# Kernel tuning notes

Measured on AMD Instinct MI355X. Metric: run time of the kernel, lower is better.

## Reference

```python
import jax, jax.numpy as jnp
import numpy as np

D_MODEL = 1024
NHEAD = 16


def unitnorm(v):
    # F.normalize(v, dim=-1): v / max(||v||_2, 1e-12)
    n = jnp.sqrt(jnp.sum(v * v, axis=-1, keepdims=True))
    return v / jnp.maximum(n, 1e-12)


def setup_inputs() -> dict:
    key = jax.random.key(0)
    ks = jax.random.split(key, 14)
    d = D_MODEL
    sc = 1.0 / np.sqrt(d)
    inp = jax.random.normal(ks[0], (2048, 8, d), dtype=jnp.float32)
    def lin(kw, kb, out_dim):
        W = jax.random.uniform(kw, (out_dim, d), minval=-sc, maxval=sc, dtype=jnp.float32)
        b = jax.random.uniform(kb, (out_dim,), minval=-sc, maxval=sc, dtype=jnp.float32)
        return W, b
    Wq_w, Wq_b = lin(ks[1], ks[2], d)
    Wk_w, Wk_b = lin(ks[3], ks[4], d)
    Wv_w, Wv_b = lin(ks[5], ks[6], d)
    Wo_w, Wo_b = lin(ks[7], ks[8], d)
    Ww_w, Ww_b = lin(ks[9], ks[10], NHEAD)
    Wr_w, Wr_b = lin(ks[11], ks[12], NHEAD)
    return {"inp": inp, "Wq_w": Wq_w, "Wq_b": Wq_b, "Wk_w": Wk_w, "Wk_b": Wk_b,
            "Wv_w": Wv_w, "Wv_b": Wv_b, "Wo_w": Wo_w, "Wo_b": Wo_b,
            "Ww_w": Ww_w, "Ww_b": Ww_b, "Wr_w": Wr_w, "Wr_b": Wr_b}


def reference(inp, Wq_w, Wq_b, Wk_w, Wk_b, Wv_w, Wv_b, Wo_w, Wo_b, Ww_w, Ww_b, Wr_w, Wr_b):
    src = inp  # src=None path
    S, B, d = inp.shape
    n = NHEAD
    # torch Linear: x @ W.T + b
    k = (src @ Wk_w.T + Wk_b).reshape(S, B, n, -1)
    v = (src @ Wv_w.T + Wv_b).reshape(S, B, n, -1)
    q = (inp @ Wq_w.T + Wq_b).reshape(S, B, n, -1)
    k = unitnorm(k)
    q = unitnorm(q)
    w = jax.nn.sigmoid(src @ Ww_w.T + Ww_b)            # [S,B,n]
    A = jnp.einsum('sbnq,sbnv->bnvq', k, v * w[:, :, :, None])
    r = jax.nn.sigmoid(inp @ Wr_w.T + Wr_b)            # [S,B,n]
    out = jnp.einsum('sbnq,bnvq->sbnv', q, A) * r[:, :, :, None]
    out = out.reshape(S, B, d)
    out = out @ Wo_w.T + Wo_b
    return (out, A)
```

## Files before the change

### kernel.cpp

```cpp
#include <hip/hip_runtime.h>
#include <cstdint>
#include <cstddef>


typedef __bf16 bf16x8 __attribute__((ext_vector_type(8)));
typedef float  f32x4  __attribute__((ext_vector_type(4)));
typedef unsigned short u16x8 __attribute__((ext_vector_type(8)));
typedef unsigned short u16x4 __attribute__((ext_vector_type(4)));

#define ROWS 16384
#define DM   1024

__device__ __forceinline__ unsigned short f2bf(float f) {
  unsigned int u = __builtin_bit_cast(unsigned int, f);
  u += 0x7FFFu + ((u >> 16) & 1u);
  return (unsigned short)(u >> 16);
}
__device__ __forceinline__ float bf2f(unsigned short h) {
  unsigned int u = ((unsigned int)h) << 16;
  return __builtin_bit_cast(float, u);
}
__device__ __forceinline__ float sigm(float x) { return 1.0f / (1.0f + __expf(-x)); }

__device__ __forceinline__ void gload_lds16(const void* g, void* l) {
  __builtin_amdgcn_global_load_lds((__attribute__((address_space(1))) void*)(g),
                                   (__attribute__((address_space(3))) void*)(l),
                                   16, 0, 0);
}

__global__ __launch_bounds__(256) void k_cast_x(const float* __restrict__ X,
                                                unsigned short* __restrict__ Xb) {
  size_t i = ((size_t)blockIdx.x * 256 + threadIdx.x) * 8;
  f32x4 a = *(const f32x4*)(X + i);
  f32x4 b = *(const f32x4*)(X + i + 4);
  u16x8 o;
  o[0] = f2bf(a[0]); o[1] = f2bf(a[1]); o[2] = f2bf(a[2]); o[3] = f2bf(a[3]);
  o[4] = f2bf(b[0]); o[5] = f2bf(b[1]); o[6] = f2bf(b[2]); o[7] = f2bf(b[3]);
  *(u16x8*)(Xb + i) = o;
}

__global__ __launch_bounds__(256) void k_pack_w(
    const float* __restrict__ Wq, const float* __restrict__ Wk, const float* __restrict__ Wv,
    const float* __restrict__ Wo, const float* __restrict__ Ww, const float* __restrict__ Wr,
    const float* __restrict__ bq, const float* __restrict__ bk, const float* __restrict__ bv,
    const float* __restrict__ bw, const float* __restrict__ br,
    unsigned short* __restrict__ Wpack, float* __restrict__ biasP,
    unsigned short* __restrict__ WRw, float* __restrict__ biasWR,
    unsigned short* __restrict__ Wob) {
  int r = blockIdx.x, t = threadIdx.x;
  const float* src; float bias = 0.0f; unsigned short* dst; float* bdst;
  if (r < 1024)      { src = Wq + (size_t)r * DM;          bias = bq[r];        dst = Wpack + (size_t)r * DM;          bdst = biasP + r; }
  else if (r < 2048) { src = Wk + (size_t)(r - 1024) * DM; bias = bk[r - 1024]; dst = Wpack + (size_t)r * DM;          bdst = biasP + r; }
  else if (r < 3072) { src = Wv + (size_t)(r - 2048) * DM; bias = bv[r - 2048]; dst = Wpack + (size_t)r * DM;          bdst = biasP + r; }
  else if (r < 3088) { src = Ww + (size_t)(r - 3072) * DM; bias = bw[r - 3072]; dst = WRw + (size_t)(r - 3072) * DM;   bdst = biasWR + (r - 3072); }
  else if (r < 3104) { src = Wr + (size_t)(r - 3088) * DM; bias = br[r - 3088]; dst = WRw + (size_t)(r - 3072) * DM;   bdst = biasWR + (r - 3072); }
  else               { src = Wo + (size_t)(r - 3104) * DM;                      dst = Wob + (size_t)(r - 3104) * DM;   bdst = nullptr; }
  int c = t * 4;
  f32x4 v = *(const f32x4*)(src + c);
  u16x4 o;
  o[0] = f2bf(v[0]); o[1] = f2bf(v[1]); o[2] = f2bf(v[2]); o[3] = f2bf(v[3]);
  *(u16x4*)(dst + c) = o;
  if (t == 0 && bdst) *bdst = bias;
}

__global__ __launch_bounds__(256) void k_wr(const unsigned short* __restrict__ Xb,
                                            const unsigned short* __restrict__ WRw,
                                            const float* __restrict__ biasWR,
                                            float* __restrict__ WRf) {
  __shared__ __bf16 sA[128 * 64];
  __shared__ __bf16 sB[32 * 64];
  int t = threadIdx.x, lane = t & 63, wid = t >> 6;
  int m0 = blockIdx.x * 128;
  int l15 = lane & 15, l4 = lane >> 4;
  f32x4 acc[2][2];
#pragma unroll
  for (int i = 0; i < 2; ++i)
#pragma unroll
    for (int j = 0; j < 2; ++j) acc[i][j] = (f32x4){0.f, 0.f, 0.f, 0.f};
  int srow = t >> 3, schunk = (t & 7) * 8;
  for (int kt = 0; kt < DM; kt += 64) {
#pragma unroll
    for (int c = 0; c < 4; ++c)
      gload_lds16(Xb + (size_t)(m0 + c * 32 + srow) * DM + kt + schunk,
                  (void*)(sA + c * 2048 + wid * 512));
    gload_lds16(WRw + (size_t)srow * DM + kt + schunk, (void*)(sB + wid * 512));
    __syncthreads();
#pragma unroll
    for (int ks = 0; ks < 2; ++ks) {
      bf16x8 fa[2], fb[2];
#pragma unroll
      for (int mi = 0; mi < 2; ++mi)
        fa[mi] = *(const bf16x8*)(sA + (wid * 32 + mi * 16 + l15) * 64 + (ks * 4 + l4) * 8);
#pragma unroll
      for (int ni = 0; ni < 2; ++ni)
        fb[ni] = *(const bf16x8*)(sB + (ni * 16 + l15) * 64 + (ks * 4 + l4) * 8);
#pragma unroll
      for (int mi = 0; mi < 2; ++mi)
#pragma unroll
        for (int ni = 0; ni < 2; ++ni)
          acc[mi][ni] = __builtin_amdgcn_mfma_f32_16x16x32_bf16(fa[mi], fb[ni], acc[mi][ni], 0, 0, 0);
    }
    __syncthreads();
  }
#pragma unroll
  for (int mi = 0; mi < 2; ++mi)
#pragma unroll
    for (int e = 0; e < 4; ++e) {
      int row = m0 + wid * 32 + mi * 16 + 4 * l4 + e;
#pragma unroll
      for (int ni = 0; ni < 2; ++ni)
        WRf[(size_t)row * 32 + ni * 16 + l15] = acc[mi][ni][e] + biasWR[ni * 16 + l15];
    }
}

__global__ __launch_bounds__(512, 2) void k_gemm_qkv3(
    const unsigned short* __restrict__ Xb, const unsigned short* __restrict__ Wpack,
    const float* __restrict__ biasP, const float* __restrict__ WRf,
    unsigned short* __restrict__ Qb, unsigned short* __restrict__ Kb,
    unsigned short* __restrict__ Vb) {
  __shared__ __bf16 sm[65536];
  const int t = threadIdx.x, lane = t & 63, w = t >> 6;
  const int wm = w >> 2, wn = w & 3;
  const int l15 = lane & 15, l4 = lane >> 4, l7 = lane & 7;
  int orig = blockIdx.x;
  int wg = (orig & 7) * 96 + (orig >> 3);
  const int m0 = (wg & 63) << 8;
  const int n0 = (wg >> 6) << 8;

  const int srow = t >> 3;
  const int schunk = ((t & 7) ^ (srow & 7)) * 8;
  const unsigned short* Asrc = Xb + (size_t)(m0 + srow) * DM + schunk;
  const unsigned short* Bsrc = Wpack + (size_t)(n0 + srow) * DM + schunk;

  f32x4 acc[8][4];
#pragma unroll
  for (int i = 0; i < 8; ++i)
#pragma unroll
    for (int j = 0; j < 4; ++j) acc[i][j] = (f32x4){0.f, 0.f, 0.f, 0.f};

#define STAGE256(P, kt)                                                            \
  do {                                                                             \
    _Pragma("unroll") for (int c = 0; c < 4; ++c)                                  \
      gload_lds16(Asrc + (size_t)c * 64 * DM + (kt),                               \
                  (void*)(sm + (P) * 32768 + c * 4096 + w * 512));                 \
    _Pragma("unroll") for (int c = 0; c < 4; ++c)                                  \
      gload_lds16(Bsrc + (size_t)c * 64 * DM + (kt),                               \
                  (void*)(sm + (P) * 32768 + 16384 + c * 4096 + w * 512));         \
  } while (0)

  STAGE256(0, 0);
  __syncthreads();
  for (int kt16 = 0; kt16 < 16; ++kt16) {
    int P = kt16 & 1;
    if (kt16 < 15) STAGE256(P ^ 1, (kt16 + 1) * 64);
    const __bf16* A0 = sm + P * 32768;
    const __bf16* B0 = A0 + 16384;
#pragma unroll
    for (int ks = 0; ks < 2; ++ks) {
      bf16x8 fa[8], fb[4];
      int ck = (((ks * 4 + l4) ^ l7) << 3);
#pragma unroll
      for (int mi = 0; mi < 8; ++mi)
        fa[mi] = *(const bf16x8*)(A0 + (wm * 128 + mi * 16 + l15) * 64 + ck);
#pragma unroll
      for (int ni = 0; ni < 4; ++ni)
        fb[ni] = *(const bf16x8*)(B0 + (wn * 64 + ni * 16 + l15) * 64 + ck);
#pragma unroll
      for (int mi = 0; mi < 8; ++mi)
#pragma unroll
        for (int ni = 0; ni < 4; ++ni)
          acc[mi][ni] = __builtin_amdgcn_mfma_f32_16x16x32_bf16(fa[mi], fb[ni], acc[mi][ni], 0, 0, 0);
    }
    __syncthreads();
  }
#undef STAGE256

  const int colbase = n0 + wn * 64;
  float bb[4];
#pragma unroll
  for (int ni = 0; ni < 4; ++ni) bb[ni] = biasP[colbase + ni * 16 + l15];

  if (colbase < 2048) {
    unsigned short* dstp = (colbase < 1024) ? Qb : Kb;
    int coff = (colbase < 1024) ? colbase : (colbase - 1024);
#pragma unroll
    for (int mi = 0; mi < 8; ++mi)
#pragma unroll
      for (int e = 0; e < 4; ++e) {
        float v[4]; float ssq = 0.f;
#pragma unroll
        for (int ni = 0; ni < 4; ++ni) { v[ni] = acc[mi][ni][e] + bb[ni]; ssq += v[ni] * v[ni]; }
        ssq += __shfl_xor(ssq, 1);
        ssq += __shfl_xor(ssq, 2);
        ssq += __shfl_xor(ssq, 4);
        ssq += __shfl_xor(ssq, 8);
        float sc = 1.0f / fmaxf(sqrtf(ssq), 1e-12f);
        int row = m0 + wm * 128 + mi * 16 + 4 * l4 + e;
#pragma unroll
        for (int ni = 0; ni < 4; ++ni)
          dstp[(size_t)row * DM + coff + ni * 16 + l15] = f2bf(v[ni] * sc);
      }
  } else {
    int hv = (colbase - 2048) >> 6;
    int coff = colbase - 2048;
#pragma unroll
    for (int mi = 0; mi < 8; ++mi)
#pragma unroll
      for (int e = 0; e < 4; ++e) {
        int row = m0 + wm * 128 + mi * 16 + 4 * l4 + e;
        float wgt = sigm(WRf[(size_t)row * 32 + hv]);
#pragma unroll
        for (int ni = 0; ni < 4; ++ni)
          Vb[(size_t)row * DM + coff + ni * 16 + l15] = f2bf((acc[mi][ni][e] + bb[ni]) * wgt);
      }
  }
}

__global__ __launch_bounds__(256, 2) void k_gemm_A(const unsigned short* __restrict__ Kb,
                                                   const unsigned short* __restrict__ Vb,
                                                   float* __restrict__ Apart) {
  __shared__ __bf16 sK[64 * 64];
  __shared__ __bf16 sV[64 * 64];
  int t = threadIdx.x, lane = t & 63, wid = t >> 6;
  int bn = blockIdx.x & 127, sk = blockIdx.x >> 7;
  int b = bn >> 4, n = bn & 15;
  f32x4 acc[4];
#pragma unroll
  for (int j = 0; j < 4; j++) acc[j] = (f32x4){0.f, 0.f, 0.f, 0.f};
  int lrow = lane >> 3, lcol = (lane & 7) * 8;

  for (int st = sk * 1024; st < (sk + 1) * 1024; st += 64) {
#pragma unroll
    for (int c = 0; c < 2; c++) {
      int r0 = wid * 16 + c * 8;
      size_t g = ((size_t)(st + r0 + lrow) * 8 + b) * DM + n * 64 + lcol;
      gload_lds16(Kb + g, (void*)(sK + r0 * 64));
      gload_lds16(Vb + g, (void*)(sV + r0 * 64));
    }
    __syncthreads();
#pragma unroll
    for (int kk = 0; kk < 64; kk += 32) {
      bf16x8 av, bv[4];
#pragma unroll
      for (int e = 0; e < 8; e++)
        av[e] = sV[(kk + 8 * (lane >> 4) + e) * 64 + wid * 16 + (lane & 15)];
#pragma unroll
      for (int jn = 0; jn < 4; jn++)
#pragma unroll
        for (int e = 0; e < 8; e++)
          bv[jn][e] = sK[(kk + 8 * (lane >> 4) + e) * 64 + jn * 16 + (lane & 15)];
#pragma unroll
      for (int jn = 0; jn < 4; jn++)
        acc[jn] = __builtin_amdgcn_mfma_f32_16x16x32_bf16(av, bv[jn], acc[jn], 0, 0, 0);
    }
    __syncthreads();
  }
  float* Ap = Apart + (size_t)(sk * 128 + bn) * 4096;
#pragma unroll
  for (int jn = 0; jn < 4; jn++) {
#pragma unroll
    for (int e = 0; e < 4; e++) {
      int i = wid * 16 + 4 * (lane >> 4) + e;
      int j = jn * 16 + (lane & 15);
      Ap[i * 64 + j] = acc[jn][e];
    }
  }
}

__global__ __launch_bounds__(256) void k_reduceA(const float* __restrict__ Apart,
                                                 float* __restrict__ Aout,
                                                 unsigned short* __restrict__ Abf) {
  int bn = blockIdx.x, t = threadIdx.x;
  size_t base = (size_t)bn * 4096 + t * 16;
#pragma unroll
  for (int j = 0; j < 4; ++j) {
    f32x4 x = *(const f32x4*)(Apart + base + j * 4);
    f32x4 y = *(const f32x4*)(Apart + (size_t)128 * 4096 + base + j * 4);
    x += y;
    *(f32x4*)(Aout + base + j * 4) = x;
    u16x4 o;
    o[0] = f2bf(x[0]); o[1] = f2bf(x[1]); o[2] = f2bf(x[2]); o[3] = f2bf(x[3]);
    *(u16x4*)(Abf + base + j * 4) = o;
  }
}

__global__ __launch_bounds__(256, 2) void k_gemm_o2(const unsigned short* __restrict__ Qb,
                                                    const unsigned short* __restrict__ Abf,
                                                    const float* __restrict__ WRf,
                                                    unsigned short* __restrict__ Ob) {
  __shared__ __bf16 sQ[128 * 64];
  __shared__ __bf16 sA[64 * 64];
  int t = threadIdx.x, lane = t & 63, wid = t >> 6;
  int bn = blockIdx.x & 127, stile = blockIdx.x >> 7;
  int b = bn >> 4, n = bn & 15;
  int s0 = stile * 128;
  int lrow = lane >> 3, lcol = (lane & 7) * 8;
#pragma unroll
  for (int c = 0; c < 4; c++) {
    int r0 = wid * 32 + c * 8;
    gload_lds16(Qb + ((size_t)(s0 + r0 + lrow) * 8 + b) * DM + n * 64 + lcol,
                (void*)(sQ + r0 * 64));
  }
#pragma unroll
  for (int c = 0; c < 2; c++) {
    int r0 = wid * 16 + c * 8;
    gload_lds16(Abf + (size_t)bn * 4096 + (size_t)(r0 + lrow) * 64 + lcol,
                (void*)(sA + r0 * 64));
  }
  __syncthreads();
  f32x4 acc[2][4];
#pragma unroll
  for (int i = 0; i < 2; i++)
#pragma unroll
    for (int j = 0; j < 4; j++) acc[i][j] = (f32x4){0.f, 0.f, 0.f, 0.f};
#pragma unroll
  for (int kk = 0; kk < 64; kk += 32) {
    bf16x8 aq[2], bA[4];
#pragma unroll
    for (int mi = 0; mi < 2; mi++)
      aq[mi] = *(const bf16x8*)(sQ + (wid * 32 + mi * 16 + (lane & 15)) * 64 + kk + 8 * (lane >> 4));
#pragma unroll
    for (int ni = 0; ni < 4; ni++)
      bA[ni] = *(const bf16x8*)(sA + (ni * 16 + (lane & 15)) * 64 + kk + 8 * (lane >> 4));
#pragma unroll
    for (int mi = 0; mi < 2; mi++)
#pragma unroll
      for (int ni = 0; ni < 4; ni++)
        acc[mi][ni] = __builtin_amdgcn_mfma_f32_16x16x32_bf16(aq[mi], bA[ni], acc[mi][ni], 0, 0, 0);
  }
#pragma unroll
  for (int mi = 0; mi < 2; mi++) {
#pragma unroll
    for (int e = 0; e < 4; e++) {
      int srow = wid * 32 + mi * 16 + 4 * (lane >> 4) + e;
      size_t row = (size_t)(s0 + srow) * 8 + b;
      float rv = sigm(WRf[row * 32 + 16 + n]);
#pragma unroll
      for (int ni = 0; ni < 4; ni++)
        Ob[row * DM + n * 64 + ni * 16 + (lane & 15)] = f2bf(acc[mi][ni][e] * rv);
    }
  }
}

__global__ __launch_bounds__(256, 2) void k_gemm_out(const unsigned short* __restrict__ Ob,
                                                     const unsigned short* __restrict__ Wob,
                                                     const float* __restrict__ bo,
                                                     float* __restrict__ Out) {
  __shared__ __bf16 smA[128 * 64];
  __shared__ __bf16 smB[128 * 64];
  int t = threadIdx.x, lane = t & 63, wid = t >> 6;
  int m0 = (blockIdx.x & 127) * 128;
  int n0 = (blockIdx.x >> 7) * 128;
  int wr = wid >> 1, wc = wid & 1;
  f32x4 acc[4][4];
#pragma unroll
  for (int i = 0; i < 4; i++)
#pragma unroll
    for (int j = 0; j < 4; j++) acc[i][j] = (f32x4){0.f, 0.f, 0.f, 0.f};
  int srow = wid * 32;
  int lrow = lane >> 3, lcol = (lane & 7) * 8;

  for (int kt = 0; kt < DM; kt += 64) {
#pragma unroll
    for (int c = 0; c < 4; c++) {
      int r = srow + c * 8 + lrow;
      gload_lds16(Ob + (size_t)(m0 + r) * DM + kt + lcol, (void*)(smA + (srow + c * 8) * 64));
      gload_lds16(Wob + (size_t)(n0 + r) * DM + kt + lcol, (void*)(smB + (srow + c * 8) * 64));
    }
    __syncthreads();
#pragma unroll
    for (int kk = 0; kk < 64; kk += 32) {
      bf16x8 fa[4], fb[4];
#pragma unroll
      for (int mi = 0; mi < 4; mi++)
        fa[mi] = *(const bf16x8*)(smA + (wr * 64 + mi * 16 + (lane & 15)) * 64 + kk + 8 * (lane >> 4));
#pragma unroll
      for (int ni = 0; ni < 4; ni++)
        fb[ni] = *(const bf16x8*)(smB + (wc * 64 + ni * 16 + (lane & 15)) * 64 + kk + 8 * (lane >> 4));
#pragma unroll
      for (int mi = 0; mi < 4; mi++)
#pragma unroll
        for (int ni = 0; ni < 4; ni++)
          acc[mi][ni] = __builtin_amdgcn_mfma_f32_16x16x32_bf16(fa[mi], fb[ni], acc[mi][ni], 0, 0, 0);
    }
    __syncthreads();
  }
#pragma unroll
  for (int mi = 0; mi < 4; mi++) {
#pragma unroll
    for (int e = 0; e < 4; e++) {
      int row = m0 + wr * 64 + mi * 16 + 4 * (lane >> 4) + e;
#pragma unroll
      for (int ni = 0; ni < 4; ni++) {
        int col = n0 + wc * 64 + ni * 16 + (lane & 15);
        Out[(size_t)row * DM + col] = acc[mi][ni][e] + bo[col];
      }
    }
  }
}

extern "C" void kernel_launch(void* const* d_in, const int* in_sizes, int n_in,
                              void* d_out, int out_size, void* d_ws, size_t ws_size,
                              hipStream_t stream) {
  (void)in_sizes; (void)n_in; (void)out_size; (void)ws_size;
  const float* X  = (const float*)d_in[0];
  const float* Wq = (const float*)d_in[1];  const float* bq = (const float*)d_in[2];
  const float* Wk = (const float*)d_in[3];  const float* bk = (const float*)d_in[4];
  const float* Wv = (const float*)d_in[5];  const float* bv = (const float*)d_in[6];
  const float* Wo = (const float*)d_in[7];  const float* bo = (const float*)d_in[8];
  const float* Ww = (const float*)d_in[9];  const float* bw = (const float*)d_in[10];
  const float* Wr = (const float*)d_in[11]; const float* br = (const float*)d_in[12];

  char* ws = (char*)d_ws;
  unsigned short* Wpack = (unsigned short*)(ws + 0);
  float*          Apart = (float*)(ws + 0);
  unsigned short* Abf   = (unsigned short*)(ws + 4194304);
  float*          biasP = (float*)(ws + 6291456);
  unsigned short* WRw   = (unsigned short*)(ws + 6303744);
  float*          biasWR= (float*)(ws + 6369280);
  unsigned short* Wob   = (unsigned short*)(ws + 6369408);
  unsigned short* Xb    = (unsigned short*)(ws + 8466560);
  unsigned short* Ob    = Xb;
  unsigned short* Qb    = (unsigned short*)(ws + 42020992);
  unsigned short* Kb    = (unsigned short*)(ws + 75575424);
  unsigned short* Vb    = (unsigned short*)(ws + 109129856);
  float*          WRf   = (float*)(ws + 142684288);

  float* Out0 = (float*)d_out;
  float* Aout = Out0 + (size_t)ROWS * DM;

  k_cast_x<<<dim3(8192), dim3(256), 0, stream>>>(X, Xb);
  k_pack_w<<<dim3(4128), dim3(256), 0, stream>>>(Wq, Wk, Wv, Wo, Ww, Wr,
                                                 bq, bk, bv, bw, br,
                                                 Wpack, biasP, WRw, biasWR, Wob);
  k_wr<<<dim3(128), dim3(256), 0, stream>>>(Xb, WRw, biasWR, WRf);
  k_gemm_qkv3<<<dim3(768), dim3(512), 0, stream>>>(Xb, Wpack, biasP, WRf, Qb, Kb, Vb);
  k_gemm_A<<<dim3(256), dim3(256), 0, stream>>>(Kb, Vb, Apart);
  k_reduceA<<<dim3(128), dim3(256), 0, stream>>>(Apart, Aout, Abf);
  k_gemm_o2<<<dim3(2048), dim3(256), 0, stream>>>(Qb, Abf, WRf, Ob);
  k_gemm_out<<<dim3(1024), dim3(256), 0, stream>>>(Ob, Wob, bo, Out0);
}
```

Baseline: 250.1 us.

## Add 8-phase pipelined 256x256 GEMM core for QKV and output projections

Result: slower. 407.5 us (+63.0%).

```diff
diff --git a/kernel.cpp b/kernel.cpp
--- a/kernel.cpp
+++ b/kernel.cpp
@@ -113,7 +113,140 @@
     }
 }
 
-__global__ __launch_bounds__(512, 2) void k_gemm_qkv3(
+
+__device__ __forceinline__ void stage_a(const unsigned short* __restrict__ Ag, int m0, int kt,
+                                        __bf16* sm, int P, int H, int lane, int w) {
+#pragma unroll
+  for (int e = 0; e < 2; ++e) {
+    int i  = e * 64 + w * 8 + (lane >> 3);
+    int jp = (lane & 7) ^ (lane >> 3);
+    int grow = m0 + ((i >> 6) << 7) + H * 64 + (i & 63);
+    gload_lds16(Ag + (size_t)grow * DM + kt + jp * 8,
+                (void*)(sm + P * 16384 + H * 8192 + (e * 64 + w * 8) * 64));
+  }
+}
+__device__ __forceinline__ void stage_b(const unsigned short* __restrict__ Bg, int n0, int kt,
+                                        __bf16* sm, int P, int H, int lane, int w) {
+#pragma unroll
+  for (int e = 0; e < 2; ++e) {
+    int i  = e * 64 + w * 8 + (lane >> 3);
+    int jp = (lane & 7) ^ (lane >> 3);
+    int grow = n0 + ((i >> 5) << 6) + H * 32 + (i & 31);
+    gload_lds16(Bg + (size_t)grow * DM + kt + jp * 8,
+                (void*)(sm + 32768 + P * 16384 + H * 8192 + (e * 64 + w * 8) * 64));
+  }
+}
+
+__device__ __forceinline__ void rd_a8(bf16x8 (&dst)[4][2], const __bf16* sm, int P, int H,
+                                      int wm, int l15, int l4, int l7) {
+#pragma unroll
+  for (int mi = 0; mi < 4; ++mi)
+#pragma unroll
+    for (int ks = 0; ks < 2; ++ks)
+      dst[mi][ks] = *(const bf16x8*)(sm + P * 16384 + H * 8192
+          + (wm * 64 + mi * 16 + l15) * 64 + (((ks * 4 + l4) ^ l7) << 3));
+}
+__device__ __forceinline__ void rd_b4(bf16x8 (&dst)[2][2], const __bf16* sm, int P, int H,
+                                      int wn, int l15, int l4, int l7) {
+#pragma unroll
+  for (int ni = 0; ni < 2; ++ni)
+#pragma unroll
+    for (int ks = 0; ks < 2; ++ks)
+      dst[ni][ks] = *(const bf16x8*)(sm + 32768 + P * 16384 + H * 8192
+          + (wn * 32 + ni * 16 + l15) * 64 + (((ks * 4 + l4) ^ l7) << 3));
+}
+
+#define MFMA16(MH, NV)                                                              \
+  _Pragma("unroll") for (int ks = 0; ks < 2; ++ks)                                  \
+  _Pragma("unroll") for (int mi = 0; mi < 4; ++mi)                                  \
+  _Pragma("unroll") for (int ni = 0; ni < 2; ++ni)                                  \
+    acc[(MH) * 4 + mi][(NV) * 2 + ni] = __builtin_amdgcn_mfma_f32_16x16x32_bf16(    \
+        fa[MH][mi][ks], fb[NV][ni][ks], acc[(MH) * 4 + mi][(NV) * 2 + ni], 0, 0, 0)
+
+#define PH8(RD, LGKM, STG, MH, NV, CP)                                              \
+  do {                                                                              \
+    RD; STG;                                                                        \
+    __builtin_amdgcn_s_barrier();                                                   \
+    asm volatile("s_waitcnt lgkmcnt(" #LGKM ")" ::: "memory");                      \
+    __builtin_amdgcn_sched_barrier(0);                                              \
+    __builtin_amdgcn_s_setprio(1);                                                  \
+    MFMA16(MH, NV);                                                                 \
+    __builtin_amdgcn_s_setprio(0);                                                  \
+    __builtin_amdgcn_sched_barrier(0);                                              \
+    CP;                                                                             \
+    __builtin_amdgcn_s_barrier();                                                   \
+  } while (0)
+
+#define VMW(N) asm volatile("s_waitcnt vmcnt(" #N ")" ::: "memory")
+
+template <int MODE>
+__device__ __forceinline__ void iter8(const unsigned short* __restrict__ Ag,
+                                      const unsigned short* __restrict__ Bg,
+                                      __bf16* sm, f32x4 (&acc)[8][4],
+                                      bf16x8 (&fa)[2][4][2], bf16x8 (&fb)[2][2][2],
+                                      int m0, int n0, int lane, int w, int wm, int wn,
+                                      int l15, int l4, int l7, int k2, int k3, int k4) {
+  PH8(rd_b4(fb[1], sm, 0, 1, wn, l15, l4, l7), 4,
+      if (MODE < 2) stage_b(Bg, n0, k2, sm, 0, 0, lane, w), 0, 0, (void)0);
+  PH8(rd_a8(fa[1], sm, 0, 1, wm, l15, l4, l7), 8,
+      if (MODE < 2) stage_b(Bg, n0, k2, sm, 0, 1, lane, w), 0, 1, (void)0);
+  PH8(rd_a8(fa[0], sm, 1, 0, wm, l15, l4, l7), 8,
+      if (MODE < 2) stage_a(Ag, m0, k2, sm, 0, 1, lane, w), 1, 0, (void)0);
+  PH8(rd_b4(fb[0], sm, 1, 0, wn, l15, l4, l7), 4,
+      if (MODE < 2) stage_a(Ag, m0, k3, sm, 1, 0, lane, w), 1, 1,
+      if (MODE == 2) { VMW(0); } else { VMW(6); });
+  PH8(rd_b4(fb[1], sm, 1, 1, wn, l15, l4, l7), 4,
+      if (MODE < 2) stage_b(Bg, n0, k3, sm, 1, 0, lane, w), 0, 0, (void)0);
+  PH8(rd_a8(fa[1], sm, 1, 1, wm, l15, l4, l7), 8,
+      if (MODE < 2) stage_b(Bg, n0, k3, sm, 1, 1, lane, w), 0, 1, (void)0);
+  if (MODE < 2) {
+    PH8(rd_a8(fa[0], sm, 0, 0, wm, l15, l4, l7), 8,
+        stage_a(Ag, m0, k3, sm, 1, 1, lane, w), 1, 0, (void)0);
+  } else {
+    PH8((void)0, 0, (void)0, 1, 0, (void)0);
+  }
+  if (MODE == 0) {
+    PH8(rd_b4(fb[0], sm, 0, 0, wn, l15, l4, l7), 4,
+        stage_a(Ag, m0, k4, sm, 0, 0, lane, w), 1, 1, VMW(6));
+  } else if (MODE == 1) {
+    PH8(rd_b4(fb[0], sm, 0, 0, wn, l15, l4, l7), 4, (void)0, 1, 1, VMW(4));
+  } else {
+    PH8((void)0, 0, (void)0, 1, 1, (void)0);
+  }
+}
+
+__device__ __forceinline__ void gemm256_8p(const unsigned short* __restrict__ Ag,
+                                           const unsigned short* __restrict__ Bg,
+                                           __bf16* sm, f32x4 (&acc)[8][4],
+                                           int m0, int n0, int lane, int w) {
+  const int wm = w >> 2, wn = w & 3;
+  const int l15 = lane & 15, l4 = lane >> 4, l7 = lane & 7;
+  bf16x8 fa[2][4][2];
+  bf16x8 fb[2][2][2];
+  stage_a(Ag, m0, 0, sm, 0, 0, lane, w);
+  stage_a(Ag, m0, 0, sm, 0, 1, lane, w);
+  stage_b(Bg, n0, 0, sm, 0, 0, lane, w);
+  stage_b(Bg, n0, 0, sm, 0, 1, lane, w);
+  stage_a(Ag, m0, 64, sm, 1, 0, lane, w);
+  stage_a(Ag, m0, 64, sm, 1, 1, lane, w);
+  stage_b(Bg, n0, 64, sm, 1, 0, lane, w);
+  stage_b(Bg, n0, 64, sm, 1, 1, lane, w);
+  VMW(8);
+  __builtin_amdgcn_s_barrier();
+  rd_a8(fa[0], sm, 0, 0, wm, l15, l4, l7);
+  rd_b4(fb[0], sm, 0, 0, wn, l15, l4, l7);
+  asm volatile("s_waitcnt lgkmcnt(0)" ::: "memory");
+  __builtin_amdgcn_sched_barrier(0);
+  __builtin_amdgcn_s_barrier();
+  stage_a(Ag, m0, 128, sm, 0, 0, lane, w);
+  for (int i = 0; i < 6; ++i)
+    iter8<0>(Ag, Bg, sm, acc, fa, fb, m0, n0, lane, w, wm, wn, l15, l4, l7,
+             (2 * i + 2) * 64, (2 * i + 3) * 64, (2 * i + 4) * 64);
+  iter8<1>(Ag, Bg, sm, acc, fa, fb, m0, n0, lane, w, wm, wn, l15, l4, l7, 896, 960, 0);
+  iter8<2>(Ag, Bg, sm, acc, fa, fb, m0, n0, lane, w, wm, wn, l15, l4, l7, 0, 0, 0);
+}
+
+__global__ __launch_bounds__(512, 2) void k_gemm_qkv4(
     const unsigned short* __restrict__ Xb, const unsigned short* __restrict__ Wpack,
     const float* __restrict__ biasP, const float* __restrict__ WRf,
     unsigned short* __restrict__ Qb, unsigned short* __restrict__ Kb,
@@ -121,99 +254,113 @@
   __shared__ __bf16 sm[65536];
   const int t = threadIdx.x, lane = t & 63, w = t >> 6;
   const int wm = w >> 2, wn = w & 3;
-  const int l15 = lane & 15, l4 = lane >> 4, l7 = lane & 7;
+  const int l15 = lane & 15, l4 = lane >> 4;
   int orig = blockIdx.x;
   int wg = (orig & 7) * 96 + (orig >> 3);
   const int m0 = (wg & 63) << 8;
   const int n0 = (wg >> 6) << 8;
-
-  const int srow = t >> 3;
-  const int schunk = ((t & 7) ^ (srow & 7)) * 8;
-  const unsigned short* Asrc = Xb + (size_t)(m0 + srow) * DM + schunk;
-  const unsigned short* Bsrc = Wpack + (size_t)(n0 + srow) * DM + schunk;
-
   f32x4 acc[8][4];
 #pragma unroll
   for (int i = 0; i < 8; ++i)
 #pragma unroll
     for (int j = 0; j < 4; ++j) acc[i][j] = (f32x4){0.f, 0.f, 0.f, 0.f};
-
-#define STAGE256(P, kt)                                                            \
-  do {                                                                             \
-    _Pragma("unroll") for (int c = 0; c < 4; ++c)                                  \
-      gload_lds16(Asrc + (size_t)c * 64 * DM + (kt),                               \
-                  (void*)(sm + (P) * 32768 + c * 4096 + w * 512));                 \
-    _Pragma("unroll") for (int c = 0; c < 4; ++c)                                  \
-      gload_lds16(Bsrc + (size_t)c * 64 * DM + (kt),                               \
-                  (void*)(sm + (P) * 32768 + 16384 + c * 4096 + w * 512));         \
-  } while (0)
-
-  STAGE256(0, 0);
-  __syncthreads();
-  for (int kt16 = 0; kt16 < 16; ++kt16) {
-    int P = kt16 & 1;
-    if (kt16 < 15) STAGE256(P ^ 1, (kt16 + 1) * 64);
-    const __bf16* A0 = sm + P * 32768;
-    const __bf16* B0 = A0 + 16384;
-#pragma unroll
-    for (int ks = 0; ks < 2; ++ks) {
-      bf16x8 fa[8], fb[4];
-      int ck = (((ks * 4 + l4) ^ l7) << 3);
-#pragma unroll
-      for (int mi = 0; mi < 8; ++mi)
-        fa[mi] = *(const bf16x8*)(A0 + (wm * 128 + mi * 16 + l15) * 64 + ck);
-#pragma unroll
-      for (int ni = 0; ni < 4; ++ni)
-        fb[ni] = *(const bf16x8*)(B0 + (wn * 64 + ni * 16 + l15) * 64 + ck);
-#pragma unroll
-      for (int mi = 0; mi < 8; ++mi)
-#pragma unroll
-        for (int ni = 0; ni < 4; ++ni)
-          acc[mi][ni] = __builtin_amdgcn_mfma_f32_16x16x32_bf16(fa[mi], fb[ni], acc[mi][ni], 0, 0, 0);
-    }
-    __syncthreads();
-  }
-#undef STAGE256
+  gemm256_8p(Xb, Wpack, sm, acc, m0, n0, lane, w);
 
   const int colbase = n0 + wn * 64;
-  float bb[4];
-#pragma unroll
-  for (int ni = 0; ni < 4; ++ni) bb[ni] = biasP[colbase + ni * 16 + l15];
+  float bb[2][2];
+#pragma unroll
+  for (int nv = 0; nv < 2; ++nv)
+#pragma unroll
+    for (int ni = 0; ni < 2; ++ni) bb[nv][ni] = biasP[colbase + nv * 32 + ni * 16 + l15];
 
   if (colbase < 2048) {
     unsigned short* dstp = (colbase < 1024) ? Qb : Kb;
     int coff = (colbase < 1024) ? colbase : (colbase - 1024);
 #pragma unroll
-    for (int mi = 0; mi < 8; ++mi)
-#pragma unroll
-      for (int e = 0; e < 4; ++e) {
-        float v[4]; float ssq = 0.f;
-#pragma unroll
-        for (int ni = 0; ni < 4; ++ni) { v[ni] = acc[mi][ni][e] + bb[ni]; ssq += v[ni] * v[ni]; }
-        ssq += __shfl_xor(ssq, 1);
-        ssq += __shfl_xor(ssq, 2);
-        ssq += __shfl_xor(ssq, 4);
-        ssq += __shfl_xor(ssq, 8);
-        float sc = 1.0f / fmaxf(sqrtf(ssq), 1e-12f);
-        int row = m0 + wm * 128 + mi * 16 + 4 * l4 + e;
-#pragma unroll
-        for (int ni = 0; ni < 4; ++ni)
-          dstp[(size_t)row * DM + coff + ni * 16 + l15] = f2bf(v[ni] * sc);
-      }
+    for (int mh = 0; mh < 2; ++mh)
+#pragma unroll
+      for (int mi = 0; mi < 4; ++mi)
+#pragma unroll
+        for (int e = 0; e < 4; ++e) {
+          float v[2][2]; float ssq = 0.f;
+#pragma unroll
+          for (int nv = 0; nv < 2; ++nv)
+#pragma unroll
+            for (int ni = 0; ni < 2; ++ni) {
+              v[nv][ni] = acc[mh * 4 + mi][nv * 2 + ni][e] + bb[nv][ni];
+              ssq += v[nv][ni] * v[nv][ni];
+            }
+          ssq += __shfl_xor(ssq, 1);
+          ssq += __shfl_xor(ssq, 2);
+          ssq += __shfl_xor(ssq, 4);
+          ssq += __shfl_xor(ssq, 8);
+          float sc = 1.0f / fmaxf(sqrtf(ssq), 1e-12f);
+          int row = m0 + wm * 128 + mh * 64 + mi * 16 + 4 * l4 + e;
+#pragma unroll
+          for (int nv = 0; nv < 2; ++nv)
+#pragma unroll
+            for (int ni = 0; ni < 2; ++ni)
+              dstp[(size_t)row * DM + coff + nv * 32 + ni * 16 + l15] = f2bf(v[nv][ni] * sc);
+        }
   } else {
     int hv = (colbase - 2048) >> 6;
     int coff = colbase - 2048;
 #pragma unroll
-    for (int mi = 0; mi < 8; ++mi)
+    for (int mh = 0; mh < 2; ++mh)
+#pragma unroll
+      for (int mi = 0; mi < 4; ++mi)
+#pragma unroll
+        for (int e = 0; e < 4; ++e) {
+          int row = m0 + wm * 128 + mh * 64 + mi * 16 + 4 * l4 + e;
+          float wgt = sigm(WRf[(size_t)row * 32 + hv]);
+#pragma unroll
+          for (int nv = 0; nv < 2; ++nv)
+#pragma unroll
+            for (int ni = 0; ni < 2; ++ni)
+              Vb[(size_t)row * DM + coff + nv * 32 + ni * 16 + l15] =
+                  f2bf((acc[mh * 4 + mi][nv * 2 + ni][e] + bb[nv][ni]) * wgt);
+        }
+  }
+}
+
+__global__ __launch_bounds__(512, 2) void k_gemm_out4(
+    const unsigned short* __restrict__ Ob, const unsigned short* __restrict__ Wob,
+    const float* __restrict__ bo, float* __restrict__ Out) {
+  __shared__ __bf16 sm[65536];
+  const int t = threadIdx.x, lane = t & 63, w = t >> 6;
+  const int wm = w >> 2, wn = w & 3;
+  const int l15 = lane & 15, l4 = lane >> 4;
+  int orig = blockIdx.x;
+  int wg = (orig & 7) * 32 + (orig >> 3);
+  const int m0 = (wg & 63) << 8;
+  const int n0 = (wg >> 6) << 8;
+  f32x4 acc[8][4];
+#pragma unroll
+  for (int i = 0; i < 8; ++i)
+#pragma unroll
+    for (int j = 0; j < 4; ++j) acc[i][j] = (f32x4){0.f, 0.f, 0.f, 0.f};
+  gemm256_8p(Ob, Wob, sm, acc, m0, n0, lane, w);
+
+  float bb[2][2];
+#pragma unroll
+  for (int nv = 0; nv < 2; ++nv)
+#pragma unroll
+    for (int ni = 0; ni < 2; ++ni) bb[nv][ni] = bo[n0 + wn * 64 + nv * 32 + ni * 16 + l15];
+#pragma unroll
+  for (int mh = 0; mh < 2; ++mh)
+#pragma unroll
+    for (int mi = 0; mi < 4; ++mi)
 #pragma unroll
       for (int e = 0; e < 4; ++e) {
-        int row = m0 + wm * 128 + mi * 16 + 4 * l4 + e;
-        float wgt = sigm(WRf[(size_t)row * 32 + hv]);
-#pragma unroll
-        for (int ni = 0; ni < 4; ++ni)
-          Vb[(size_t)row * DM + coff + ni * 16 + l15] = f2bf((acc[mi][ni][e] + bb[ni]) * wgt);
+        int row = m0 + wm * 128 + mh * 64 + mi * 16 + 4 * l4 + e;
+#pragma unroll
+        for (int nv = 0; nv < 2; ++nv)
+#pragma unroll
+          for (int ni = 0; ni < 2; ++ni) {
+            int col = n0 + wn * 64 + nv * 32 + ni * 16 + l15;
+            Out[(size_t)row * DM + col] = acc[mh * 4 + mi][nv * 2 + ni][e] + bb[nv][ni];
+          }
       }
-  }
 }
 
 __global__ __launch_bounds__(256, 2) void k_gemm_A(const unsigned short* __restrict__ Kb,
@@ -338,63 +485,6 @@
 #pragma unroll
       for (int ni = 0; ni < 4; ni++)
         Ob[row * DM + n * 64 + ni * 16 + (lane & 15)] = f2bf(acc[mi][ni][e] * rv);
-    }
-  }
-}
-
-__global__ __launch_bounds__(256, 2) void k_gemm_out(const unsigned short* __restrict__ Ob,
-                                                     const unsigned short* __restrict__ Wob,
-                                                     const float* __restrict__ bo,
-                                                     float* __restrict__ Out) {
-  __shared__ __bf16 smA[128 * 64];
-  __shared__ __bf16 smB[128 * 64];
-  int t = threadIdx.x, lane = t & 63, wid = t >> 6;
-  int m0 = (blockIdx.x & 127) * 128;
-  int n0 = (blockIdx.x >> 7) * 128;
-  int wr = wid >> 1, wc = wid & 1;
-  f32x4 acc[4][4];
-#pragma unroll
-  for (int i = 0; i < 4; i++)
-#pragma unroll
-    for (int j = 0; j < 4; j++) acc[i][j] = (f32x4){0.f, 0.f, 0.f, 0.f};
-  int srow = wid * 32;
-  int lrow = lane >> 3, lcol = (lane & 7) * 8;
-
-  for (int kt = 0; kt < DM; kt += 64) {
-#pragma unroll
-    for (int c = 0; c < 4; c++) {
-      int r = srow + c * 8 + lrow;
-      gload_lds16(Ob + (size_t)(m0 + r) * DM + kt + lcol, (void*)(smA + (srow + c * 8) * 64));
-      gload_lds16(Wob + (size_t)(n0 + r) * DM + kt + lcol, (void*)(smB + (srow + c * 8) * 64));
-    }
-    __syncthreads();
-#pragma unroll
-    for (int kk = 0; kk < 64; kk += 32) {
-      bf16x8 fa[4], fb[4];
-#pragma unroll
-      for (int mi = 0; mi < 4; mi++)
-        fa[mi] = *(const bf16x8*)(smA + (wr * 64 + mi * 16 + (lane & 15)) * 64 + kk + 8 * (lane >> 4));
-#pragma unroll
-      for (int ni = 0; ni < 4; ni++)
-        fb[ni] = *(const bf16x8*)(smB + (wc * 64 + ni * 16 + (lane & 15)) * 64 + kk + 8 * (lane >> 4));
-#pragma unroll
-      for (int mi = 0; mi < 4; mi++)
-#pragma unroll
-        for (int ni = 0; ni < 4; ni++)
-          acc[mi][ni] = __builtin_amdgcn_mfma_f32_16x16x32_bf16(fa[mi], fb[ni], acc[mi][ni], 0, 0, 0);
-    }
-    __syncthreads();
-  }
-#pragma unroll
-  for (int mi = 0; mi < 4; mi++) {
-#pragma unroll
-    for (int e = 0; e < 4; e++) {
-      int row = m0 + wr * 64 + mi * 16 + 4 * (lane >> 4) + e;
-#pragma unroll
-      for (int ni = 0; ni < 4; ni++) {
-        int col = n0 + wc * 64 + ni * 16 + (lane & 15);
-        Out[(size_t)row * DM + col] = acc[mi][ni][e] + bo[col];
-      }
     }
   }
 }
@@ -434,9 +524,9 @@
                                                  bq, bk, bv, bw, br,
                                                  Wpack, biasP, WRw, biasWR, Wob);
   k_wr<<<dim3(128), dim3(256), 0, stream>>>(Xb, WRw, biasWR, WRf);
-  k_gemm_qkv3<<<dim3(768), dim3(512), 0, stream>>>(Xb, Wpack, biasP, WRf, Qb, Kb, Vb);
+  k_gemm_qkv4<<<dim3(768), dim3(512), 0, stream>>>(Xb, Wpack, biasP, WRf, Qb, Kb, Vb);
   k_gemm_A<<<dim3(256), dim3(256), 0, stream>>>(Kb, Vb, Apart);
   k_reduceA<<<dim3(128), dim3(256), 0, stream>>>(Apart, Aout, Abf);
   k_gemm_o2<<<dim3(2048), dim3(256), 0, stream>>>(Qb, Abf, WRf, Ob);
-  k_gemm_out<<<dim3(1024), dim3(256), 0, stream>>>(Ob, Wob, bo, Out0);
-}
+  k_gemm_out4<<<dim3(256), dim3(512), 0, stream>>>(Ob, Wob, bo, Out0);
+}
```

## Use shared triple-buffered K32 pipeline for QKV and output GEMMs

Applied to the files above, without the earlier changes.

After: 246.8 us. Within noise of the previous version (-1.3%).

```diff
diff --git a/kernel.cpp b/kernel.cpp
--- a/kernel.cpp
+++ b/kernel.cpp
@@ -113,67 +113,107 @@
     }
 }
 
-__global__ __launch_bounds__(512, 2) void k_gemm_qkv3(
+
+#define VMW(N) asm volatile("s_waitcnt vmcnt(" #N ")" ::: "memory")
+#define LGKM0  asm volatile("s_waitcnt lgkmcnt(0)" ::: "memory")
+#define SB0    __builtin_amdgcn_sched_barrier(0)
+
+__device__ __forceinline__ void stage3(const unsigned short* __restrict__ Asrc,
+                                       const unsigned short* __restrict__ Bsrc,
+                                       int kt, __bf16* sm, int rbase, int w) {
+#pragma unroll
+  for (int c = 0; c < 2; ++c)
+    gload_lds16(Asrc + (size_t)c * 128 * DM + kt, (void*)(sm + rbase + c * 4096 + w * 512));
+#pragma unroll
+  for (int c = 0; c < 2; ++c)
+    gload_lds16(Bsrc + (size_t)c * 128 * DM + kt, (void*)(sm + rbase + 8192 + c * 4096 + w * 512));
+}
+
+__device__ __forceinline__ void comp3(const __bf16* base, f32x4 (&acc)[8][4],
+                                      const int (&aoff)[8], const int (&boff)[4]) {
+  bf16x8 fa[8], fb[4];
+#pragma unroll
+  for (int mi = 0; mi < 8; ++mi) fa[mi] = *(const bf16x8*)(base + aoff[mi]);
+#pragma unroll
+  for (int ni = 0; ni < 4; ++ni) fb[ni] = *(const bf16x8*)(base + boff[ni]);
+  LGKM0; SB0;
+  __builtin_amdgcn_s_setprio(1);
+#pragma unroll
+  for (int mi = 0; mi < 8; ++mi)
+#pragma unroll
+    for (int ni = 0; ni < 4; ++ni)
+      acc[mi][ni] = __builtin_amdgcn_mfma_f32_16x16x32_bf16(fa[mi], fb[ni], acc[mi][ni], 0, 0, 0);
+  __builtin_amdgcn_s_setprio(0);
+  SB0;
+}
+
+__device__ __forceinline__ void gemm_d3(const unsigned short* __restrict__ Ag,
+                                        const unsigned short* __restrict__ Bg,
+                                        __bf16* sm, f32x4 (&acc)[8][4],
+                                        int m0, int n0, int lane, int w) {
+  const int wm = w >> 2, wn = w & 3;
+  const int l15 = lane & 15, l4 = lane >> 4;
+  const int t = w * 64 + lane;
+  const int srow = t >> 2;
+  const int schunk = ((t & 3) ^ (srow & 3)) * 8;
+  const unsigned short* Asrc = Ag + (size_t)(m0 + srow) * DM + schunk;
+  const unsigned short* Bsrc = Bg + (size_t)(n0 + srow) * DM + schunk;
+
+  int aoff[8], boff[4];
+#pragma unroll
+  for (int mi = 0; mi < 8; ++mi) {
+    int r = wm * 128 + mi * 16 + l15;
+    aoff[mi] = r * 32 + ((l4 ^ (r & 3)) << 3);
+  }
+#pragma unroll
+  for (int ni = 0; ni < 4; ++ni) {
+    int r = wn * 64 + ni * 16 + l15;
+    boff[ni] = 8192 + r * 32 + ((l4 ^ (r & 3)) << 3);
+  }
+
+  stage3(Asrc, Bsrc, 0, sm, 0, w);
+  stage3(Asrc, Bsrc, 32, sm, 16384, w);
+  VMW(4);
+  __builtin_amdgcn_s_barrier();
+  SB0;
+
+  int rdb = 0, stb = 32768;
+  for (int it = 0; it < 30; ++it) {
+    stage3(Asrc, Bsrc, (it + 2) * 32, sm, stb, w);
+    comp3(sm + rdb, acc, aoff, boff);
+    VMW(4);
+    __builtin_amdgcn_s_barrier();
+    SB0;
+    rdb += 16384; if (rdb == 49152) rdb = 0;
+    stb += 16384; if (stb == 49152) stb = 0;
+  }
+  comp3(sm + rdb, acc, aoff, boff);
+  VMW(0);
+  __builtin_amdgcn_s_barrier();
+  SB0;
+  rdb += 16384; if (rdb == 49152) rdb = 0;
+  comp3(sm + rdb, acc, aoff, boff);
+}
+
+__global__ __launch_bounds__(512, 2) void k_gemm_qkv5(
     const unsigned short* __restrict__ Xb, const unsigned short* __restrict__ Wpack,
     const float* __restrict__ biasP, const float* __restrict__ WRf,
     unsigned short* __restrict__ Qb, unsigned short* __restrict__ Kb,
     unsigned short* __restrict__ Vb) {
-  __shared__ __bf16 sm[65536];
+  __shared__ __bf16 sm[49152];
   const int t = threadIdx.x, lane = t & 63, w = t >> 6;
   const int wm = w >> 2, wn = w & 3;
-  const int l15 = lane & 15, l4 = lane >> 4, l7 = lane & 7;
+  const int l15 = lane & 15, l4 = lane >> 4;
   int orig = blockIdx.x;
   int wg = (orig & 7) * 96 + (orig >> 3);
   const int m0 = (wg & 63) << 8;
   const int n0 = (wg >> 6) << 8;
-
-  const int srow = t >> 3;
-  const int schunk = ((t & 7) ^ (srow & 7)) * 8;
-  const unsigned short* Asrc = Xb + (size_t)(m0 + srow) * DM + schunk;
-  const unsigned short* Bsrc = Wpack + (size_t)(n0 + srow) * DM + schunk;
-
   f32x4 acc[8][4];
 #pragma unroll
   for (int i = 0; i < 8; ++i)
 #pragma unroll
     for (int j = 0; j < 4; ++j) acc[i][j] = (f32x4){0.f, 0.f, 0.f, 0.f};
-
-#define STAGE256(P, kt)                                                            \
-  do {                                                                             \
-    _Pragma("unroll") for (int c = 0; c < 4; ++c)                                  \
-      gload_lds16(Asrc + (size_t)c * 64 * DM + (kt),                               \
-                  (void*)(sm + (P) * 32768 + c * 4096 + w * 512));                 \
-    _Pragma("unroll") for (int c = 0; c < 4; ++c)                                  \
-      gload_lds16(Bsrc + (size_t)c * 64 * DM + (kt),                               \
-                  (void*)(sm + (P) * 32768 + 16384 + c * 4096 + w * 512));         \
-  } while (0)
-
-  STAGE256(0, 0);
-  __syncthreads();
-  for (int kt16 = 0; kt16 < 16; ++kt16) {
-    int P = kt16 & 1;
-    if (kt16 < 15) STAGE256(P ^ 1, (kt16 + 1) * 64);
-    const __bf16* A0 = sm + P * 32768;
-    const __bf16* B0 = A0 + 16384;
-#pragma unroll
-    for (int ks = 0; ks < 2; ++ks) {
-      bf16x8 fa[8], fb[4];
-      int ck = (((ks * 4 + l4) ^ l7) << 3);
-#pragma unroll
-      for (int mi = 0; mi < 8; ++mi)
-        fa[mi] = *(const bf16x8*)(A0 + (wm * 128 + mi * 16 + l15) * 64 + ck);
-#pragma unroll
-      for (int ni = 0; ni < 4; ++ni)
-        fb[ni] = *(const bf16x8*)(B0 + (wn * 64 + ni * 16 + l15) * 64 + ck);
-#pragma unroll
-      for (int mi = 0; mi < 8; ++mi)
-#pragma unroll
-        for (int ni = 0; ni < 4; ++ni)
-          acc[mi][ni] = __builtin_amdgcn_mfma_f32_16x16x32_bf16(fa[mi], fb[ni], acc[mi][ni], 0, 0, 0);
-    }
-    __syncthreads();
-  }
-#undef STAGE256
+  gemm_d3(Xb, Wpack, sm, acc, m0, n0, lane, w);
 
   const int colbase = n0 + wn * 64;
   float bb[4];
@@ -214,6 +254,40 @@
           Vb[(size_t)row * DM + coff + ni * 16 + l15] = f2bf((acc[mi][ni][e] + bb[ni]) * wgt);
       }
   }
+}
+
+__global__ __launch_bounds__(512, 2) void k_gemm_out5(
+    const unsigned short* __restrict__ Ob, const unsigned short* __restrict__ Wob,
+    const float* __restrict__ bo, float* __restrict__ Out) {
+  __shared__ __bf16 sm[49152];
+  const int t = threadIdx.x, lane = t & 63, w = t >> 6;
+  const int wm = w >> 2, wn = w & 3;
+  const int l15 = lane & 15, l4 = lane >> 4;
+  int orig = blockIdx.x;
+  int wg = (orig & 7) * 32 + (orig >> 3);
+  const int m0 = (wg & 63) << 8;
+  const int n0 = (wg >> 6) << 8;
+  f32x4 acc[8][4];
+#pragma unroll
+  for (int i = 0; i < 8; ++i)
+#pragma unroll
+    for (int j = 0; j < 4; ++j) acc[i][j] = (f32x4){0.f, 0.f, 0.f, 0.f};
+  gemm_d3(Ob, Wob, sm, acc, m0, n0, lane, w);
+
+  float bb[4];
+#pragma unroll
+  for (int ni = 0; ni < 4; ++ni) bb[ni] = bo[n0 + wn * 64 + ni * 16 + l15];
+#pragma unroll
+  for (int mi = 0; mi < 8; ++mi)
+#pragma unroll
+    for (int e = 0; e < 4; ++e) {
+      int row = m0 + wm * 128 + mi * 16 + 4 * l4 + e;
+#pragma unroll
+      for (int ni = 0; ni < 4; ++ni) {
+        int col = n0 + wn * 64 + ni * 16 + l15;
+        Out[(size_t)row * DM + col] = acc[mi][ni][e] + bb[ni];
+      }
+    }
 }
 
 __global__ __launch_bounds__(256, 2) void k_gemm_A(const unsigned short* __restrict__ Kb,
@@ -338,63 +412,6 @@
 #pragma unroll
       for (int ni = 0; ni < 4; ni++)
         Ob[row * DM + n * 64 + ni * 16 + (lane & 15)] = f2bf(acc[mi][ni][e] * rv);
-    }
-  }
-}
-
-__global__ __launch_bounds__(256, 2) void k_gemm_out(const unsigned short* __restrict__ Ob,
-                                                     const unsigned short* __restrict__ Wob,
-                                                     const float* __restrict__ bo,
-                                                     float* __restrict__ Out) {
-  __shared__ __bf16 smA[128 * 64];
-  __shared__ __bf16 smB[128 * 64];
-  int t = threadIdx.x, lane = t & 63, wid = t >> 6;
-  int m0 = (blockIdx.x & 127) * 128;
-  int n0 = (blockIdx.x >> 7) * 128;
-  int wr = wid >> 1, wc = wid & 1;
-  f32x4 acc[4][4];
-#pragma unroll
-  for (int i = 0; i < 4; i++)
-#pragma unroll
-    for (int j = 0; j < 4; j++) acc[i][j] = (f32x4){0.f, 0.f, 0.f, 0.f};
-  int srow = wid * 32;
-  int lrow = lane >> 3, lcol = (lane & 7) * 8;
-
-  for (int kt = 0; kt < DM; kt += 64) {
-#pragma unroll
-    for (int c = 0; c < 4; c++) {
-      int r = srow + c * 8 + lrow;
-      gload_lds16(Ob + (size_t)(m0 + r) * DM + kt + lcol, (void*)(smA + (srow + c * 8) * 64));
-      gload_lds16(Wob + (size_t)(n0 + r) * DM + kt + lcol, (void*)(smB + (srow + c * 8) * 64));
-    }
-    __syncthreads();
-#pragma unroll
-    for (int kk = 0; kk < 64; kk += 32) {
-      bf16x8 fa[4], fb[4];
-#pragma unroll
-      for (int mi = 0; mi < 4; mi++)
-        fa[mi] = *(const bf16x8*)(smA + (wr * 64 + mi * 16 + (lane & 15)) * 64 + kk + 8 * (lane >> 4));
-#pragma unroll
-      for (int ni = 0; ni < 4; ni++)
-        fb[ni] = *(const bf16x8*)(smB + (wc * 64 + ni * 16 + (lane & 15)) * 64 + kk + 8 * (lane >> 4));
-#pragma unroll
-      for (int mi = 0; mi < 4; mi++)
-#pragma unroll
-        for (int ni = 0; ni < 4; ni++)
-          acc[mi][ni] = __builtin_amdgcn_mfma_f32_16x16x32_bf16(fa[mi], fb[ni], acc[mi][ni], 0, 0, 0);
-    }
-    __syncthreads();
-  }
-#pragma unroll
-  for (int mi = 0; mi < 4; mi++) {
-#pragma unroll
-    for (int e = 0; e < 4; e++) {
-      int row = m0 + wr * 64 + mi * 16 + 4 * (lane >> 4) + e;
-#pragma unroll
-      for (int ni = 0; ni < 4; ni++) {
-        int col = n0 + wc * 64 + ni * 16 + (lane & 15);
-        Out[(size_t)row * DM + col] = acc[mi][ni][e] + bo[col];
-      }
     }
   }
 }
@@ -434,9 +451,9 @@
                                                  bq, bk, bv, bw, br,
                                                  Wpack, biasP, WRw, biasWR, Wob);
   k_wr<<<dim3(128), dim3(256), 0, stream>>>(Xb, WRw, biasWR, WRf);
-  k_gemm_qkv3<<<dim3(768), dim3(512), 0, stream>>>(Xb, Wpack, biasP, WRf, Qb, Kb, Vb);
+  k_gemm_qkv5<<<dim3(768), dim3(512), 0, stream>>>(Xb, Wpack, biasP, WRf, Qb, Kb, Vb);
   k_gemm_A<<<dim3(256), dim3(256), 0, stream>>>(Kb, Vb, Apart);
   k_reduceA<<<dim3(128), dim3(256), 0, stream>>>(Apart, Aout, Abf);
   k_gemm_o2<<<dim3(2048), dim3(256), 0, stream>>>(Qb, Abf, WRf, Ob);
-  k_gemm_out<<<dim3(1024), dim3(256), 0, stream>>>(Ob, Wob, bo, Out0);
-}
+  k_gemm_out5<<<dim3(256), dim3(512), 0, stream>>>(Ob, Wob, bo, Out0);
+}
```
